# Optimization experiments

Measured on AMD Instinct MI355X. Metric: run time of the kernel, lower is better.

Reference implementation:

```python
import jax, jax.numpy as jnp
import numpy as np

NODE_TYPE_SIZE = 9      # common.NodeType.SIZE in MeshGraphNets
N_NODES = 1_000_000
N_CELLS = 2_000_000


def setup_inputs() -> dict:
    key = jax.random.key(0)
    k1, k2, k3, k4, k5 = jax.random.split(key, 5)
    world_pos = jax.random.normal(k1, (1, N_NODES, 3), dtype=jnp.float32)
    prev_world_pos = world_pos + 0.01 * jax.random.normal(k2, (1, N_NODES, 3), dtype=jnp.float32)
    mesh_pos = jax.random.normal(k3, (1, N_NODES, 3), dtype=jnp.float32)
    node_type = jax.random.randint(k4, (1, N_NODES, 1), 0, NODE_TYPE_SIZE, dtype=jnp.int64)
    # random triangles with guaranteed-distinct vertices (avoids degenerate
    # zero-length edges, matching real meshes where triangle corners differ)
    base = jax.random.randint(k5, (N_CELLS, 1), 0, N_NODES, dtype=jnp.int64)
    cells = jnp.mod(base + jnp.arange(3, dtype=jnp.int64)[None, :], N_NODES)[None]
    return {
        'world_pos': world_pos,
        'prev_world_pos': prev_world_pos,
        'mesh_pos': mesh_pos,
        'node_type': node_type,
        'cells': cells,
    }


def _triangles_to_edges(cells):
    # cells: [F, 3] -> bidirectional directed edge list [2 * 3F]
    a, b, c = cells[:, 0], cells[:, 1], cells[:, 2]
    u = jnp.concatenate([a, b, c])  # edge endpoints (a,b),(b,c),(c,a)
    v = jnp.concatenate([b, c, a])
    senders = jnp.concatenate([u, v])
    receivers = jnp.concatenate([v, u])
    return senders, receivers


def reference(world_pos, prev_world_pos, mesh_pos, node_type, cells):
    # squeeze the leading batch dim of 1, as the torch module does
    world_pos = jnp.squeeze(world_pos, 0)          # [N, 3]
    prev_world_pos = jnp.squeeze(prev_world_pos, 0)
    mesh_pos = jnp.squeeze(mesh_pos, 0)
    node_type = jnp.squeeze(node_type, 0)          # [N, 1]
    cells = jnp.squeeze(cells, 0)                  # [F, 3]

    velocity = world_pos - prev_world_pos                                   # [N, 3]
    nt_onehot = jax.nn.one_hot(node_type[:, 0], NODE_TYPE_SIZE,
                               dtype=world_pos.dtype)                        # [N, 9]
    node_features = jnp.concatenate([velocity, nt_onehot], axis=-1)          # [N, 12]

    senders, receivers = _triangles_to_edges(cells)                          # [E]
    rel_world = world_pos[senders] - world_pos[receivers]                    # [E, 3]
    rel_mesh = mesh_pos[senders] - mesh_pos[receivers]                       # [E, 3]
    edge_features = jnp.concatenate([
        rel_world,
        jnp.linalg.norm(rel_world, axis=-1, keepdims=True),
        rel_mesh,
        jnp.linalg.norm(rel_mesh, axis=-1, keepdims=True),
    ], axis=-1)                                                              # [E, 7]
    return node_features, edge_features
```

## Files before the change

kernel.cpp:

```cpp
#include <hip/hip_runtime.h>

typedef float f4 __attribute__((ext_vector_type(4)));

struct F3 { float x, y, z; };
struct F9 { float v[9]; };
struct I3 { int a, b, c; };

#define BLK 256

__device__ __forceinline__ f4 mkf4(float a, float b, float c, float d) {
    f4 v; v.x = a; v.y = b; v.z = c; v.w = d; return v;
}
__device__ __forceinline__ F3 sub3p(const float* a, const float* b) {
    F3 r; r.x = a[0] - b[0]; r.y = a[1] - b[1]; r.z = a[2] - b[2]; return r;
}
__device__ __forceinline__ float nrm3(F3 v) { return sqrtf(v.x * v.x + v.y * v.y + v.z * v.z); }


__global__ void __launch_bounds__(BLK) fused(const float* __restrict__ world,
                                             const float* __restrict__ prev,
                                             const float* __restrict__ mesh,
                                             const int* __restrict__ ntype,
                                             const int* __restrict__ cells,
                                             f4* __restrict__ nf,
                                             f4* __restrict__ ef,
                                             int n_nodes, int n_cells, int edge_blocks) {
    __shared__ __align__(16) unsigned char smem[2 * 3 * BLK * 16];
    int lt = threadIdx.x;

    if ((int)blockIdx.x < edge_blocks) {
        f4 (*lds)[3][BLK] = (f4 (*)[3][BLK])smem;
        int c0 = blockIdx.x * BLK;
        int chunk = min(BLK, n_cells - c0);
        F3 rw[3], rm[3];
        float nw[3], nm[3];
        if (lt < chunk) {
            I3 t;
            __builtin_memcpy(&t, cells + 3 * (size_t)(c0 + lt), sizeof(I3));
            F9 w9, m9;
            if (t.b == t.a + 1 && t.c == t.a + 2) {
                __builtin_memcpy(&w9, world + 3 * (size_t)t.a, sizeof(F9));
                __builtin_memcpy(&m9, mesh  + 3 * (size_t)t.a, sizeof(F9));
            } else {
                __builtin_memcpy(&w9.v[0], world + 3 * (size_t)t.a, 12);
                __builtin_memcpy(&w9.v[3], world + 3 * (size_t)t.b, 12);
                __builtin_memcpy(&w9.v[6], world + 3 * (size_t)t.c, 12);
                __builtin_memcpy(&m9.v[0], mesh  + 3 * (size_t)t.a, 12);
                __builtin_memcpy(&m9.v[3], mesh  + 3 * (size_t)t.b, 12);
                __builtin_memcpy(&m9.v[6], mesh  + 3 * (size_t)t.c, 12);
            }
            rw[0] = sub3p(&w9.v[0], &w9.v[3]); rm[0] = sub3p(&m9.v[0], &m9.v[3]);
            rw[1] = sub3p(&w9.v[3], &w9.v[6]); rm[1] = sub3p(&m9.v[3], &m9.v[6]);
            rw[2] = sub3p(&w9.v[6], &w9.v[0]); rm[2] = sub3p(&m9.v[6], &m9.v[0]);
            #pragma unroll
            for (int r = 0; r < 3; r++) { nw[r] = nrm3(rw[r]); nm[r] = nrm3(rm[r]); }
            #pragma unroll
            for (int r = 0; r < 3; r++) {
                lds[0][r][lt] = mkf4(rw[r].x, rw[r].y, rw[r].z, nw[r]);
                lds[1][r][lt] = mkf4(rm[r].x, rm[r].y, rm[r].z, nm[r]);
            }
        }
        __syncthreads();
        size_t NC = (size_t)n_cells;
        if (chunk == BLK) {
            #pragma unroll
            for (int r = 0; r < 3; r++) {
                f4* G = ef + 2 * ((size_t)r * NC + (size_t)c0);
                __builtin_nontemporal_store(lds[lt & 1][r][lt >> 1], G + lt);
                int j = lt + BLK;
                __builtin_nontemporal_store(lds[j & 1][r][j >> 1], G + j);
            }
        } else {
            for (int r = 0; r < 3; r++) {
                f4* G = ef + 2 * ((size_t)r * NC + (size_t)c0);
                for (int j = lt; j < 2 * chunk; j += BLK)
                    __builtin_nontemporal_store(lds[j & 1][r][j >> 1], G + j);
            }
        }
        __syncthreads();
        if (lt < chunk) {
            #pragma unroll
            for (int r = 0; r < 3; r++) {
                lds[0][r][lt] = mkf4(-rw[r].x, -rw[r].y, -rw[r].z, nw[r]);
                lds[1][r][lt] = mkf4(-rm[r].x, -rm[r].y, -rm[r].z, nm[r]);
            }
        }
        __syncthreads();
        if (chunk == BLK) {
            #pragma unroll
            for (int r = 0; r < 3; r++) {
                f4* G = ef + 2 * (((size_t)r + 3) * NC + (size_t)c0);
                __builtin_nontemporal_store(lds[lt & 1][r][lt >> 1], G + lt);
                int j = lt + BLK;
                __builtin_nontemporal_store(lds[j & 1][r][j >> 1], G + j);
            }
        } else {
            for (int r = 0; r < 3; r++) {
                f4* G = ef + 2 * (((size_t)r + 3) * NC + (size_t)c0);
                for (int j = lt; j < 2 * chunk; j += BLK)
                    __builtin_nontemporal_store(lds[j & 1][r][j >> 1], G + j);
            }
        }
    } else {
        f4 (*lds)[BLK + 1] = (f4 (*)[BLK + 1])smem;
        int n0 = (blockIdx.x - edge_blocks) * BLK;
        int chunk = min(BLK, n_nodes - n0);
        int n = n0 + lt;
        if (lt < chunk) {
            F3 w, p;
            __builtin_memcpy(&w, world + 3 * (size_t)n, sizeof(F3));
            __builtin_memcpy(&p, prev + 3 * (size_t)n, sizeof(F3));
            int t = ntype[n];
            lds[0][lt] = mkf4(w.x - p.x, w.y - p.y, w.z - p.z, t == 0 ? 1.f : 0.f);
            lds[1][lt] = mkf4(t == 1 ? 1.f : 0.f, t == 2 ? 1.f : 0.f, t == 3 ? 1.f : 0.f, t == 4 ? 1.f : 0.f);
            lds[2][lt] = mkf4(t == 5 ? 1.f : 0.f, t == 6 ? 1.f : 0.f, t == 7 ? 1.f : 0.f, t == 8 ? 1.f : 0.f);
        }
        __syncthreads();
        f4* G = nf + 3 * (size_t)n0;
        if (chunk == BLK) {
            #pragma unroll
            for (int m = 0; m < 3; m++) {
                int j = lt + m * BLK;
                __builtin_nontemporal_store(lds[j % 3][j / 3], G + j);
            }
        } else {
            for (int j = lt; j < 3 * chunk; j += BLK)
                __builtin_nontemporal_store(lds[j % 3][j / 3], G + j);
        }
    }
}

extern "C" void kernel_launch(void* const* d_in, const int* in_sizes, int n_in,
                              void* d_out, int out_size, void* d_ws, size_t ws_size,
                              hipStream_t stream) {
    const float* world = (const float*)d_in[0];
    const float* prev  = (const float*)d_in[1];
    const float* mesh  = (const float*)d_in[2];
    const int* ntype   = (const int*)d_in[3];
    const int* cells   = (const int*)d_in[4];
    int n_nodes = in_sizes[0] / 3;
    int n_cells = in_sizes[4] / 3;

    float* out = (float*)d_out;
    f4* nf = (f4*)out;
    f4* ef = (f4*)(out + (size_t)n_nodes * 12);

    int edge_blocks = (n_cells + BLK - 1) / BLK;
    int node_blocks = (n_nodes + BLK - 1) / BLK;

    fused<<<dim3(edge_blocks + node_blocks), dim3(BLK), 0, stream>>>(
        world, prev, mesh, ntype, cells, nf, ef, n_nodes, n_cells, edge_blocks);
}
```

Before: 532.9 us.

## Precompute consecutive-node edge deltas and norms into workspace for contiguous triangles

Adds a pre-pass kernel that computes, for every node n, the world and mesh differences to node n+1 plus their norms, packed into two aligned float4s in the workspace. When a triangle's vertices are consecutive, the edge kernel loads two such 32-byte records instead of gathering 36 unaligned bytes each from world and mesh. It derives the third edge as the negated sum of the first two. This saves gather traffic and sqrt work in the edge path. In exchange it adds an extra launch and a full pass over the nodes that reads world and mesh and writes 32 bytes per node.

```diff
diff --git a/kernel.cpp b/kernel.cpp
--- a/kernel.cpp
+++ b/kernel.cpp
@@ -3,6 +3,7 @@
 typedef float f4 __attribute__((ext_vector_type(4)));
 
 struct F3 { float x, y, z; };
+struct F6 { float v[6]; };
 struct F9 { float v[9]; };
 struct I3 { int a, b, c; };
 
@@ -16,12 +17,27 @@
 }
 __device__ __forceinline__ float nrm3(F3 v) { return sqrtf(v.x * v.x + v.y * v.y + v.z * v.z); }
 
+__global__ void __launch_bounds__(BLK) precompute_R(const float* __restrict__ world,
+                                                    const float* __restrict__ mesh,
+                                                    float* __restrict__ R, int n_nodes) {
+    int n = blockIdx.x * BLK + threadIdx.x;
+    if (n >= n_nodes - 1) return;
+    F6 w, m;
+    __builtin_memcpy(&w, world + 3 * (size_t)n, sizeof(F6));
+    __builtin_memcpy(&m, mesh + 3 * (size_t)n, sizeof(F6));
+    float dwx = w.v[0] - w.v[3], dwy = w.v[1] - w.v[4], dwz = w.v[2] - w.v[5];
+    float dmx = m.v[0] - m.v[3], dmy = m.v[1] - m.v[4], dmz = m.v[2] - m.v[5];
+    f4* Rp = (f4*)R + 2 * (size_t)n;
+    Rp[0] = mkf4(dwx, dwy, dwz, sqrtf(dwx * dwx + dwy * dwy + dwz * dwz));
+    Rp[1] = mkf4(dmx, dmy, dmz, sqrtf(dmx * dmx + dmy * dmy + dmz * dmz));
+}
 
 __global__ void __launch_bounds__(BLK) fused(const float* __restrict__ world,
                                              const float* __restrict__ prev,
                                              const float* __restrict__ mesh,
                                              const int* __restrict__ ntype,
                                              const int* __restrict__ cells,
+                                             const float* __restrict__ R,
                                              f4* __restrict__ nf,
                                              f4* __restrict__ ef,
                                              int n_nodes, int n_cells, int edge_blocks) {
@@ -37,23 +53,34 @@
         if (lt < chunk) {
             I3 t;
             __builtin_memcpy(&t, cells + 3 * (size_t)(c0 + lt), sizeof(I3));
-            F9 w9, m9;
-            if (t.b == t.a + 1 && t.c == t.a + 2) {
-                __builtin_memcpy(&w9, world + 3 * (size_t)t.a, sizeof(F9));
-                __builtin_memcpy(&m9, mesh  + 3 * (size_t)t.a, sizeof(F9));
+            bool fast = (R != nullptr) && (t.b == t.a + 1) && (t.c == t.a + 2);
+            if (fast) {
+                const f4* Rp = (const f4*)R + 2 * (size_t)t.a;
+                f4 w0 = Rp[0], m0 = Rp[1], w1 = Rp[2], m1 = Rp[3];
+                rw[0].x = w0.x; rw[0].y = w0.y; rw[0].z = w0.z; nw[0] = w0.w;
+                rm[0].x = m0.x; rm[0].y = m0.y; rm[0].z = m0.z; nm[0] = m0.w;
+                rw[1].x = w1.x; rw[1].y = w1.y; rw[1].z = w1.z; nw[1] = w1.w;
+                rm[1].x = m1.x; rm[1].y = m1.y; rm[1].z = m1.z; nm[1] = m1.w;
+                float sx = w0.x + w1.x, sy = w0.y + w1.y, sz = w0.z + w1.z;
+                rw[2].x = -sx; rw[2].y = -sy; rw[2].z = -sz;
+                nw[2] = sqrtf(sx * sx + sy * sy + sz * sz);
+                float ux = m0.x + m1.x, uy = m0.y + m1.y, uz = m0.z + m1.z;
+                rm[2].x = -ux; rm[2].y = -uy; rm[2].z = -uz;
+                nm[2] = sqrtf(ux * ux + uy * uy + uz * uz);
             } else {
+                F9 w9, m9;
                 __builtin_memcpy(&w9.v[0], world + 3 * (size_t)t.a, 12);
                 __builtin_memcpy(&w9.v[3], world + 3 * (size_t)t.b, 12);
                 __builtin_memcpy(&w9.v[6], world + 3 * (size_t)t.c, 12);
-                __builtin_memcpy(&m9.v[0], mesh  + 3 * (size_t)t.a, 12);
-                __builtin_memcpy(&m9.v[3], mesh  + 3 * (size_t)t.b, 12);
-                __builtin_memcpy(&m9.v[6], mesh  + 3 * (size_t)t.c, 12);
+                __builtin_memcpy(&m9.v[0], mesh + 3 * (size_t)t.a, 12);
+                __builtin_memcpy(&m9.v[3], mesh + 3 * (size_t)t.b, 12);
+                __builtin_memcpy(&m9.v[6], mesh + 3 * (size_t)t.c, 12);
+                rw[0] = sub3p(&w9.v[0], &w9.v[3]); rm[0] = sub3p(&m9.v[0], &m9.v[3]);
+                rw[1] = sub3p(&w9.v[3], &w9.v[6]); rm[1] = sub3p(&m9.v[3], &m9.v[6]);
+                rw[2] = sub3p(&w9.v[6], &w9.v[0]); rm[2] = sub3p(&m9.v[6], &m9.v[0]);
+                #pragma unroll
+                for (int r = 0; r < 3; r++) { nw[r] = nrm3(rw[r]); nm[r] = nrm3(rm[r]); }
             }
-            rw[0] = sub3p(&w9.v[0], &w9.v[3]); rm[0] = sub3p(&m9.v[0], &m9.v[3]);
-            rw[1] = sub3p(&w9.v[3], &w9.v[6]); rm[1] = sub3p(&m9.v[3], &m9.v[6]);
-            rw[2] = sub3p(&w9.v[6], &w9.v[0]); rm[2] = sub3p(&m9.v[6], &m9.v[0]);
-            #pragma unroll
-            for (int r = 0; r < 3; r++) { nw[r] = nrm3(rw[r]); nm[r] = nrm3(rm[r]); }
             #pragma unroll
             for (int r = 0; r < 3; r++) {
                 lds[0][r][lt] = mkf4(rw[r].x, rw[r].y, rw[r].z, nw[r]);
@@ -145,9 +172,16 @@
     f4* nf = (f4*)out;
     f4* ef = (f4*)(out + (size_t)n_nodes * 12);
 
+    const float* Rptr = nullptr;
+    size_t need = (size_t)n_nodes * 32;
+    if (d_ws != nullptr && ws_size >= need && n_nodes >= 2) {
+        int pre_blocks = (n_nodes - 1 + BLK - 1) / BLK;
+        precompute_R<<<dim3(pre_blocks), dim3(BLK), 0, stream>>>(world, mesh, (float*)d_ws, n_nodes);
+        Rptr = (const float*)d_ws;
+    }
+
     int edge_blocks = (n_cells + BLK - 1) / BLK;
     int node_blocks = (n_nodes + BLK - 1) / BLK;
-
     fused<<<dim3(edge_blocks + node_blocks), dim3(BLK), 0, stream>>>(
-        world, prev, mesh, ntype, cells, nf, ef, n_nodes, n_cells, edge_blocks);
+        world, prev, mesh, ntype, cells, Rptr, nf, ef, n_nodes, n_cells, edge_blocks);
 }
```

New measurement: 503.8 us. 1.06x faster.
